# Performance work log

Measured on AMD Instinct MI355X. Metric: run time of the kernel, lower is better.

Reference implementation:

```python
import jax, jax.numpy as jnp
import numpy as np

V, E, H, T = 50000, 300, 512, 16   # vocab, embed_dim, hidden_dim, tagset
Hh = H // 2                         # per-direction LSTM hidden
B, S = 128, 128                     # batch (hardcoded in module), seq_len
START, STOP = 14, 15
NEG = -10000.0


def setup_inputs() -> dict:
    key = jax.random.key(0)
    ks = jax.random.split(key, 16)
    n = lambda k, sh: (jax.random.normal(k, sh, dtype=jnp.float32) * 0.1)
    trans = jax.random.normal(ks[12], (T, T), dtype=jnp.float32)
    trans = trans.at[START, :].set(NEG).at[:, STOP].set(NEG)
    return {
        "sentence": jax.random.randint(ks[0], (B, S), 0, V, dtype=jnp.int32),
        "emb": jax.random.normal(ks[1], (V, E), dtype=jnp.float32),
        "Wih_f": n(ks[2], (4 * Hh, E)), "Whh_f": n(ks[3], (4 * Hh, Hh)),
        "bih_f": n(ks[4], (4 * Hh,)),   "bhh_f": n(ks[5], (4 * Hh,)),
        "Wih_b": n(ks[6], (4 * Hh, E)), "Whh_b": n(ks[7], (4 * Hh, Hh)),
        "bih_b": n(ks[8], (4 * Hh,)),   "bhh_b": n(ks[9], (4 * Hh,)),
        "W_out": n(ks[10], (T, H)),     "b_out": n(ks[11], (T,)),
        "trans": trans,
        "h0": jax.random.normal(ks[13], (2, B, Hh), dtype=jnp.float32),
        "c0": jax.random.normal(ks[14], (2, B, Hh), dtype=jnp.float32),
    }


def _lstm_dir(x_sbE, h0, c0, Wih, Whh, bih, bhh):
    """x_sbE: [S,B,E] -> [S,B,Hh]. PyTorch gate order: i,f,g,o."""
    def cell(carry, xt):
        h, c = carry
        g = xt @ Wih.T + bih + h @ Whh.T + bhh
        i, f, gg, o = jnp.split(g, 4, axis=-1)
        c = jax.nn.sigmoid(f) * c + jax.nn.sigmoid(i) * jnp.tanh(gg)
        h = jax.nn.sigmoid(o) * jnp.tanh(c)
        return (h, c), h
    _, hs = jax.lax.scan(cell, (h0, c0), x_sbE)
    return hs


def _viterbi(feats, trans):
    """Batched Viterbi. feats: [B,S,T]. Returns (scores [B], paths [B,S])."""
    init = jnp.full((B, T), NEG, dtype=feats.dtype).at[:, START].set(0.0)

    def step(fv, feat_t):
        # next_tag_var[b, next, prev] = fv[b, prev] + trans[next, prev]
        nxt = fv[:, None, :] + trans[None, :, :]
        bp = jnp.argmax(nxt, axis=-1)              # [B,T]
        fv = jnp.max(nxt, axis=-1) + feat_t        # [B,T]
        return fv, bp

    fv, bps = jax.lax.scan(step, init, jnp.swapaxes(feats, 0, 1))  # bps: [S,B,T]
    term = fv + trans[STOP][None, :]
    best = jnp.argmax(term, axis=-1)               # [B]
    score = jnp.max(term, axis=-1)                 # [B]

    def back(tag, bp_t):
        prev = jnp.take_along_axis(bp_t, tag[:, None], axis=1)[:, 0]
        return prev, tag

    _, path = jax.lax.scan(back, best, bps, reverse=True)  # [S,B]
    return score, jnp.swapaxes(path, 0, 1)


def reference(sentence, emb, Wih_f, Whh_f, bih_f, bhh_f,
              Wih_b, Whh_b, bih_b, bhh_b, W_out, b_out, trans, h0, c0):
    x = emb[sentence]                               # [B,S,E] (frozen embedding)
    x_sbE = jnp.swapaxes(x, 0, 1)                   # [S,B,E]
    h_f = _lstm_dir(x_sbE, h0[0], c0[0], Wih_f, Whh_f, bih_f, bhh_f)
    h_b = _lstm_dir(x_sbE[::-1], h0[1], c0[1], Wih_b, Whh_b, bih_b, bhh_b)[::-1]
    lstm_out = jnp.concatenate([h_f, h_b], axis=-1)  # [S,B,H]
    feats = jnp.swapaxes(lstm_out @ W_out.T + b_out, 0, 1)  # [B,S,T]
    scores, tag_seqs = _viterbi(feats, trans)
    return scores, tag_seqs
```

## Files before the change

### kernel.cpp

```cpp
#include <hip/hip_runtime.h>
#include <math.h>

#define BB 128
#define SS 128
#define EE 300
#define HH 256
#define G4 1024
#define TT 16
#define NEGV -10000.0f
#define START_TAG 14
#define STOP_TAG 15

typedef float f32x4 __attribute__((ext_vector_type(4)));
typedef int   i32x4 __attribute__((ext_vector_type(4)));

__device__ __forceinline__ float sigm(float x) { return 1.0f / (1.0f + expf(-x)); }

__device__ __forceinline__ float4 shfl_xor4(float4 v, int m) {
  float4 r;
  r.x = __shfl_xor(v.x, m); r.y = __shfl_xor(v.y, m);
  r.z = __shfl_xor(v.z, m); r.w = __shfl_xor(v.w, m);
  return r;
}
__device__ __forceinline__ void add4(float4& a, const float4& b) {
  a.x += b.x; a.y += b.y; a.z += b.z; a.w += b.w;
}

__device__ __forceinline__ void load_f8_llc(const float* p, f32x4& a, f32x4& b) {
  asm volatile("global_load_dwordx4 %0, %2, off sc0 sc1\n\t"
               "global_load_dwordx4 %1, %2, off offset:16 sc0 sc1\n\t"
               "s_waitcnt vmcnt(0)"
               : "=&v"(a), "=&v"(b) : "v"(p) : "memory");
}
__device__ __forceinline__ void load_tags8(const int* p, i32x4& a, i32x4& b) {
  asm volatile("global_load_dwordx4 %0, %2, off sc0 sc1\n\t"
               "global_load_dwordx4 %1, %2, off offset:16 sc0 sc1\n\t"
               "s_waitcnt vmcnt(0)"
               : "=&v"(a), "=&v"(b) : "v"(p) : "memory");
}

__global__ void k_prep(const float* __restrict__ Wih_f, const float* __restrict__ Whh_f,
                       const float* __restrict__ bih_f, const float* __restrict__ bhh_f,
                       const float* __restrict__ Wih_b, const float* __restrict__ Whh_b,
                       const float* __restrict__ bih_b, const float* __restrict__ bhh_b,
                       float* __restrict__ WihT, float* __restrict__ Whh4,
                       float* __restrict__ bsum, int* __restrict__ ctr) {
  int id = blockIdx.x * blockDim.x + threadIdx.x;
  const int N1 = 2 * EE * G4;
  const int N2 = 2 * HH * G4;
  const int N3 = 2 * G4;
  if (id < N1) {
    int d = id / (EE * G4); int r = id % (EE * G4);
    int e = r / G4; int j = r % G4;
    const float* W = d ? Wih_b : Wih_f;
    WihT[id] = W[j * EE + e];
  } else if (id < N1 + N2) {
    int t = id - N1;
    int d = t / (HH * G4); int r = t % (HH * G4);
    int k = r / G4; int q = r % G4; int u = q >> 2; int g = q & 3;
    const float* W = d ? Whh_b : Whh_f;
    Whh4[t] = W[(g * HH + u) * HH + k];
  } else if (id < N1 + N2 + N3) {
    int t = id - N1 - N2;
    int d = t / G4; int j = t % G4;
    bsum[t] = d ? (bih_b[j] + bhh_b[j]) : (bih_f[j] + bhh_f[j]);
  } else if (id < N1 + N2 + N3 + 32 * 256) {
    ctr[id - N1 - N2 - N3] = 0;
  }
}

__global__ void k_xproj(const int* __restrict__ sent, const float* __restrict__ emb,
                        const float* __restrict__ WihT, const float* __restrict__ bsum,
                        float4* __restrict__ xp4) {
  __shared__ float xs[16][EE];
  __shared__ int idxs[16];
  int blk = blockIdx.x;
  int d = blk >> 10;
  int tile = blk & 1023;
  int tid = threadIdx.x;
  if (tid < 16) {
    int sb = tile * 16 + tid;
    int s = sb >> 7, b = sb & 127;
    idxs[tid] = sent[b * SS + s];
  }
  __syncthreads();
  for (int t = tid; t < 16 * EE; t += 256) {
    int i = t / EE, e = t % EE;
    xs[i][e] = emb[(size_t)idxs[i] * EE + e];
  }
  __syncthreads();

  const float* WT = WihT + (size_t)d * EE * G4;
  float acc0[16], acc1[16], acc2[16], acc3[16];
#pragma unroll
  for (int i = 0; i < 16; ++i) { acc0[i] = 0.f; acc1[i] = 0.f; acc2[i] = 0.f; acc3[i] = 0.f; }

  for (int e = 0; e < EE; ++e) {
    const float* row = WT + (size_t)e * G4;
    float w0 = row[tid];
    float w1 = row[tid + 256];
    float w2 = row[tid + 512];
    float w3 = row[tid + 768];
#pragma unroll
    for (int i = 0; i < 16; ++i) {
      float x = xs[i][e];
      acc0[i] += w0 * x; acc1[i] += w1 * x; acc2[i] += w2 * x; acc3[i] += w3 * x;
    }
  }
  float b0 = bsum[d * G4 + tid];
  float b1 = bsum[d * G4 + tid + 256];
  float b2 = bsum[d * G4 + tid + 512];
  float b3 = bsum[d * G4 + tid + 768];
#pragma unroll
  for (int i = 0; i < 16; ++i) {
    int sb = tile * 16 + i;
    int s = sb >> 7, b = sb & 127;
    xp4[(((size_t)d * SS + s) * BB + b) * HH + tid] =
        make_float4(acc0[i] + b0, acc1[i] + b1, acc2[i] + b2, acc3[i] + b3);
  }
}

__global__ __launch_bounds__(256, 1) void k_recur(
    const float4* __restrict__ xp4, const float4* __restrict__ Wg,
    const float* __restrict__ Wout, const float* __restrict__ h0,
    const float* __restrict__ c0, float* __restrict__ hbuf,
    float* __restrict__ featsP, int* __restrict__ ctr) {
  __shared__ __align__(16) float hshS[8 * 288];
  __shared__ float hloc[8 * 33];
  __shared__ float WoL[16 * 33];

  int blk = blockIdx.x;
  int d = blk >> 7;
  int bg = (blk >> 3) & 15;
  int sl = blk & 7;
  int bbase = bg * 8;
  int tid = threadIdx.x;
  int u = tid >> 3, kc = tid & 7;
  int uglob = sl * 32 + u;
  int* tagsg = ctr + (d * 16 + bg) * 256 + 64;

  for (int i = tid; i < 16 * 32; i += 256) {
    int t = i >> 5, uu = i & 31;
    WoL[t * 33 + uu] = Wout[t * 512 + d * HH + sl * 32 + uu];
  }

  float4 wreg[32];
  {
    const float4* Wd = Wg + (size_t)d * (HH * HH) + (size_t)(kc * 32) * HH + uglob;
#pragma unroll
    for (int kk = 0; kk < 32; ++kk) wreg[kk] = Wd[(size_t)kk * HH];
  }
  int b_own = ((kc & 1) << 2) | (kc & 2) | ((kc >> 2) & 1);
  float c_reg = c0[((size_t)d * BB + bbase + b_own) * HH + uglob];
  bool up0 = (kc & 1), up1 = (kc & 2), up2 = (kc & 4);

  float* ldst = hshS + (tid >> 5) * 288 + ((tid & 31) >> 2) * 36 + (tid & 3) * 8;

  for (int step = 0; step < SS; ++step) {
    int s = d ? (SS - 1 - step) : step;
    float4 xg = xp4[(((size_t)d * SS + s) * BB + bbase + b_own) * HH + uglob];

    if (step > 0) {
      i32x4 ta, tb;
      int m;
      do {
        load_tags8(tagsg, ta, tb);
        int m0 = min(min(ta[0], ta[1]), min(ta[2], ta[3]));
        int m1 = min(min(tb[0], tb[1]), min(tb[2], tb[3]));
        m = min(m0, m1);
      } while (m < step);
      const float* ps = hbuf + ((size_t)((step - 1) % 3) * 2 + d) * BB * HH +
                        (size_t)bbase * HH + (tid << 3);
      f32x4 a, b;
      load_f8_llc(ps, a, b);
      *(f32x4*)ldst = a;
      *(f32x4*)(ldst + 4) = b;
    } else {
      const float* ps = h0 + ((size_t)d * BB + bbase) * HH + (tid << 3);
      f32x4 a = *(const f32x4*)ps;
      f32x4 b = *(const f32x4*)(ps + 4);
      *(f32x4*)ldst = a;
      *(f32x4*)(ldst + 4) = b;
    }
    __syncthreads();

    float4 a[8];
#pragma unroll
    for (int b = 0; b < 8; ++b) a[b] = make_float4(0.f, 0.f, 0.f, 0.f);
#pragma unroll
    for (int kk4 = 0; kk4 < 8; ++kk4) {
      float hvv[8][4];
#pragma unroll
      for (int b = 0; b < 8; ++b)
        *(float4*)&hvv[b][0] = *(const float4*)&hshS[b * 288 + kc * 36 + kk4 * 4];
#pragma unroll
      for (int j = 0; j < 4; ++j) {
        float4 w = wreg[kk4 * 4 + j];
#pragma unroll
        for (int b = 0; b < 8; ++b) {
          float hj = hvv[b][j];
          a[b].x += w.x * hj; a[b].y += w.y * hj;
          a[b].z += w.z * hj; a[b].w += w.w * hj;
        }
      }
    }

#pragma unroll
    for (int j = 0; j < 4; ++j) {
      float4 snd = up0 ? a[j] : a[j + 4];
      float4 rcv = shfl_xor4(snd, 1);
      if (!up0) add4(a[j], rcv); else add4(a[j + 4], rcv);
    }
    float4 v0 = up0 ? a[4] : a[0];
    float4 v1 = up0 ? a[5] : a[1];
    float4 v2 = up0 ? a[6] : a[2];
    float4 v3 = up0 ? a[7] : a[3];
    {
      float4 snd = up1 ? v0 : v2;
      float4 rcv = shfl_xor4(snd, 2);
      if (!up1) add4(v0, rcv); else add4(v2, rcv);
      snd = up1 ? v1 : v3;
      rcv = shfl_xor4(snd, 2);
      if (!up1) add4(v1, rcv); else add4(v3, rcv);
    }
    float4 w0 = up1 ? v2 : v0;
    float4 w1 = up1 ? v3 : v1;
    {
      float4 snd = up2 ? w0 : w1;
      float4 rcv = shfl_xor4(snd, 4);
      if (!up2) add4(w0, rcv); else add4(w1, rcv);
    }
    float4 g4 = up2 ? w1 : w0;

    float ii = g4.x + xg.x, ff = g4.y + xg.y, gg = g4.z + xg.z, oo = g4.w + xg.w;
    c_reg = sigm(ff) * c_reg + sigm(ii) * tanhf(gg);
    float hn = sigm(oo) * tanhf(c_reg);

    __hip_atomic_store(
        &hbuf[((size_t)(step % 3) * 2 + d) * BB * HH + (size_t)(bbase + b_own) * HH + uglob],
        hn, __ATOMIC_RELAXED, __HIP_MEMORY_SCOPE_AGENT);
    hloc[b_own * 33 + u] = hn;
    __syncthreads();

    if (tid == 0)
      __hip_atomic_store(&tagsg[sl], step + 1, __ATOMIC_RELAXED,
                         __HIP_MEMORY_SCOPE_AGENT);

    {
      int b2 = tid >> 5, t = (tid >> 1) & 15, pr = tid & 1;
      float p = 0.f;
#pragma unroll
      for (int q = 0; q < 16; ++q)
        p += hloc[b2 * 33 + pr * 16 + q] * WoL[t * 33 + pr * 16 + q];
      p += __shfl_xor(p, 1);
      if (!pr)
        featsP[(((size_t)(d * 8 + sl) * BB + bbase + b2) * SS + s) * TT + t] = p;
    }
  }
}

__global__ void k_fsum(const float* __restrict__ featsP, float* __restrict__ featsF) {
  int b = blockIdx.x;
  int tid = threadIdx.x;
  float acc[8];
#pragma unroll
  for (int j = 0; j < 8; ++j) acc[j] = 0.f;
  for (int dsl = 0; dsl < 16; ++dsl) {
    const float* fp = featsP + ((size_t)dsl * BB + b) * (SS * TT);
#pragma unroll
    for (int j = 0; j < 8; ++j) acc[j] += fp[j * 256 + tid];
  }
  float* fo = featsF + (size_t)b * (SS * TT);
#pragma unroll
  for (int j = 0; j < 8; ++j) fo[j * 256 + tid] = acc[j];
}

__global__ void k_viterbi(const float* __restrict__ featsF, const float* __restrict__ b_out,
                          const float* __restrict__ trans, float* __restrict__ out,
                          unsigned char* __restrict__ bp) {
  __shared__ float tr[TT * TT];
  int tid = threadIdx.x;
  if (tid < TT * TT) tr[tid] = trans[tid];
  __syncthreads();

  int bg = tid >> 4;
  int next = tid & 15;
  int b = blockIdx.x * 16 + bg;
  float fv = (next == START_TAG) ? 0.0f : NEGV;
  float bo = b_out[next];
  const float* fF = featsF + (size_t)b * SS * TT;

  for (int s = 0; s < SS; ++s) {
    float best = -INFINITY; int arg = 0;
#pragma unroll
    for (int prev = 0; prev < TT; ++prev) {
      float fvp = __shfl(fv, prev, 16);
      float cand = fvp + tr[next * TT + prev];
      if (cand > best) { best = cand; arg = prev; }
    }
    float feat = fF[s * TT + next] + bo;
    fv = best + feat;
    bp[((size_t)b * SS + s) * TT + next] = (unsigned char)arg;
  }

  float bv = fv + tr[STOP_TAG * TT + next];
  int bi = next;
#pragma unroll
  for (int off = 8; off; off >>= 1) {
    float ov = __shfl_down(bv, off, 16);
    int oi = __shfl_down(bi, off, 16);
    if (ov > bv || (ov == bv && oi < bi)) { bv = ov; bi = oi; }
  }
  if (next == 0) {
    out[b] = bv;
    int tag = bi;
    float* po = out + BB + (size_t)b * SS;
    for (int s = SS - 1; s >= 0; --s) {
      po[s] = (float)tag;
      tag = bp[((size_t)b * SS + s) * TT + tag];
    }
  }
}

extern "C" void kernel_launch(void* const* d_in, const int* in_sizes, int n_in,
                              void* d_out, int out_size, void* d_ws, size_t ws_size,
                              hipStream_t stream) {
  const int*   sent  = (const int*)d_in[0];
  const float* emb   = (const float*)d_in[1];
  const float* Wih_f = (const float*)d_in[2];
  const float* Whh_f = (const float*)d_in[3];
  const float* bih_f = (const float*)d_in[4];
  const float* bhh_f = (const float*)d_in[5];
  const float* Wih_b = (const float*)d_in[6];
  const float* Whh_b = (const float*)d_in[7];
  const float* bih_b = (const float*)d_in[8];
  const float* bhh_b = (const float*)d_in[9];
  const float* Wout  = (const float*)d_in[10];
  const float* b_out = (const float*)d_in[11];
  const float* trans = (const float*)d_in[12];
  const float* h0    = (const float*)d_in[13];
  const float* c0    = (const float*)d_in[14];

  float* ws = (float*)d_ws;
  size_t off = 0;
  float* xproj  = ws + off; off += (size_t)2 * SS * BB * G4;
  float* WihT   = ws + off; off += (size_t)2 * EE * G4;
  float* Whh4   = ws + off; off += (size_t)2 * HH * G4;
  float* bsum   = ws + off; off += (size_t)2 * G4;
  float* featsP = ws + off; off += (size_t)16 * BB * SS * TT;
  float* featsF = ws + off; off += (size_t)BB * SS * TT;
  float* hbuf   = ws + off; off += (size_t)3 * 2 * BB * HH;
  int*   ctr    = (int*)(ws + off); off += 32 * 256;
  unsigned char* bp = (unsigned char*)(ws + off);

  const int NPREP = 2 * EE * G4 + 2 * HH * G4 + 2 * G4 + 32 * 256;
  k_prep<<<(NPREP + 255) / 256, 256, 0, stream>>>(Wih_f, Whh_f, bih_f, bhh_f,
                                                  Wih_b, Whh_b, bih_b, bhh_b,
                                                  WihT, Whh4, bsum, ctr);
  k_xproj<<<2048, 256, 0, stream>>>(sent, emb, WihT, bsum, (float4*)xproj);

  {
    const float4* xp4c = (const float4*)xproj;
    const float4* Wgc  = (const float4*)Whh4;
    void* kargs[] = {(void*)&xp4c, (void*)&Wgc, (void*)&Wout, (void*)&h0,
                     (void*)&c0, (void*)&hbuf, (void*)&featsP, (void*)&ctr};
    hipError_t e = hipLaunchCooperativeKernel(k_recur, dim3(256), dim3(256),
                                              kargs, 0, stream);
    if (e != hipSuccess) {
      k_recur<<<256, 256, 0, stream>>>(xp4c, Wgc, Wout, h0, c0, hbuf, featsP, ctr);
    }
  }

  k_fsum<<<BB, 256, 0, stream>>>(featsP, featsF);
  k_viterbi<<<8, 256, 0, stream>>>(featsF, b_out, trans, (float*)d_out, bp);
}
```

Measured before the change: 856.0 us.

## Split LSTM recurrence across twice as many blocks with 4 batches each

The recurrent kernel now uses 512 cooperative blocks, each handling 4 batch rows instead of 8, with launch bounds allowing two blocks per CU. This halves per-step FMA work and shuffle reduction depth per block to shorten the serial critical path. The cost is more inter-block flag traffic and duplicated weight registers. The input projection also switches to vectorized float4 embedding and shared-memory loads, and Viterbi backpointers move from global to shared memory.

```diff
diff --git a/kernel.cpp b/kernel.cpp
--- a/kernel.cpp
+++ b/kernel.cpp
@@ -1,5 +1,6 @@
 #include <hip/hip_runtime.h>
 #include <math.h>
+#include <stdint.h>
 
 #define BB 128
 #define SS 128
@@ -26,11 +27,12 @@
   a.x += b.x; a.y += b.y; a.z += b.z; a.w += b.w;
 }
 
-__device__ __forceinline__ void load_f8_llc(const float* p, f32x4& a, f32x4& b) {
-  asm volatile("global_load_dwordx4 %0, %2, off sc0 sc1\n\t"
-               "global_load_dwordx4 %1, %2, off offset:16 sc0 sc1\n\t"
+__device__ __forceinline__ f32x4 load_f4_llc(const float* p) {
+  f32x4 v;
+  asm volatile("global_load_dwordx4 %0, %1, off sc0 sc1\n\t"
                "s_waitcnt vmcnt(0)"
-               : "=&v"(a), "=&v"(b) : "v"(p) : "memory");
+               : "=v"(v) : "v"(p) : "memory");
+  return v;
 }
 __device__ __forceinline__ void load_tags8(const int* p, i32x4& a, i32x4& b) {
   asm volatile("global_load_dwordx4 %0, %2, off sc0 sc1\n\t"
@@ -49,6 +51,7 @@
   const int N1 = 2 * EE * G4;
   const int N2 = 2 * HH * G4;
   const int N3 = 2 * G4;
+  const int N4 = 64 * 256;
   if (id < N1) {
     int d = id / (EE * G4); int r = id % (EE * G4);
     int e = r / G4; int j = r % G4;
@@ -64,7 +67,7 @@
     int t = id - N1 - N2;
     int d = t / G4; int j = t % G4;
     bsum[t] = d ? (bih_b[j] + bhh_b[j]) : (bih_f[j] + bhh_f[j]);
-  } else if (id < N1 + N2 + N3 + 32 * 256) {
+  } else if (id < N1 + N2 + N3 + N4) {
     ctr[id - N1 - N2 - N3] = 0;
   }
 }
@@ -72,7 +75,7 @@
 __global__ void k_xproj(const int* __restrict__ sent, const float* __restrict__ emb,
                         const float* __restrict__ WihT, const float* __restrict__ bsum,
                         float4* __restrict__ xp4) {
-  __shared__ float xs[16][EE];
+  __shared__ __align__(16) float xs[16][EE];
   __shared__ int idxs[16];
   int blk = blockIdx.x;
   int d = blk >> 10;
@@ -84,9 +87,9 @@
     idxs[tid] = sent[b * SS + s];
   }
   __syncthreads();
-  for (int t = tid; t < 16 * EE; t += 256) {
-    int i = t / EE, e = t % EE;
-    xs[i][e] = emb[(size_t)idxs[i] * EE + e];
+  for (int t = tid; t < 16 * 75; t += 256) {
+    int i = t / 75, e4 = t % 75;
+    ((f32x4*)&xs[i][0])[e4] = ((const f32x4*)(emb + (size_t)idxs[i] * EE))[e4];
   }
   __syncthreads();
 
@@ -95,16 +98,24 @@
 #pragma unroll
   for (int i = 0; i < 16; ++i) { acc0[i] = 0.f; acc1[i] = 0.f; acc2[i] = 0.f; acc3[i] = 0.f; }
 
-  for (int e = 0; e < EE; ++e) {
-    const float* row = WT + (size_t)e * G4;
-    float w0 = row[tid];
-    float w1 = row[tid + 256];
-    float w2 = row[tid + 512];
-    float w3 = row[tid + 768];
-#pragma unroll
-    for (int i = 0; i < 16; ++i) {
-      float x = xs[i][e];
-      acc0[i] += w0 * x; acc1[i] += w1 * x; acc2[i] += w2 * x; acc3[i] += w3 * x;
+  for (int e4 = 0; e4 < 75; ++e4) {
+    f32x4 xv[16];
+#pragma unroll
+    for (int i = 0; i < 16; ++i)
+      xv[i] = *(const f32x4*)&xs[i][e4 * 4];
+    const float* rowb = WT + (size_t)e4 * 4 * G4;
+#pragma unroll
+    for (int j = 0; j < 4; ++j) {
+      const float* row = rowb + (size_t)j * G4;
+      float w0 = row[tid];
+      float w1 = row[tid + 256];
+      float w2 = row[tid + 512];
+      float w3 = row[tid + 768];
+#pragma unroll
+      for (int i = 0; i < 16; ++i) {
+        float x = xv[i][j];
+        acc0[i] += w0 * x; acc1[i] += w1 * x; acc2[i] += w2 * x; acc3[i] += w3 * x;
+      }
     }
   }
   float b0 = bsum[d * G4 + tid];
@@ -120,24 +131,24 @@
   }
 }
 
-__global__ __launch_bounds__(256, 1) void k_recur(
+__global__ __launch_bounds__(256, 2) void k_recur(
     const float4* __restrict__ xp4, const float4* __restrict__ Wg,
     const float* __restrict__ Wout, const float* __restrict__ h0,
     const float* __restrict__ c0, float* __restrict__ hbuf,
     float* __restrict__ featsP, int* __restrict__ ctr) {
-  __shared__ __align__(16) float hshS[8 * 288];
-  __shared__ float hloc[8 * 33];
+  __shared__ __align__(16) float hshS[4 * 288];
+  __shared__ float hloc[4 * 33];
   __shared__ float WoL[16 * 33];
 
   int blk = blockIdx.x;
-  int d = blk >> 7;
-  int bg = (blk >> 3) & 15;
+  int d = blk >> 8;
+  int bg = (blk >> 3) & 31;
   int sl = blk & 7;
-  int bbase = bg * 8;
+  int bbase = bg * 4;
   int tid = threadIdx.x;
   int u = tid >> 3, kc = tid & 7;
   int uglob = sl * 32 + u;
-  int* tagsg = ctr + (d * 16 + bg) * 256 + 64;
+  int* tagsg = ctr + (d * 32 + bg) * 256 + 64;
 
   for (int i = tid; i < 16 * 32; i += 256) {
     int t = i >> 5, uu = i & 31;
@@ -150,17 +161,23 @@
 #pragma unroll
     for (int kk = 0; kk < 32; ++kk) wreg[kk] = Wd[(size_t)kk * HH];
   }
-  int b_own = ((kc & 1) << 2) | (kc & 2) | ((kc >> 2) & 1);
+  int b_own = ((kc & 1) << 1) | ((kc >> 1) & 1);
   float c_reg = c0[((size_t)d * BB + bbase + b_own) * HH + uglob];
-  bool up0 = (kc & 1), up1 = (kc & 2), up2 = (kc & 4);
-
-  float* ldst = hshS + (tid >> 5) * 288 + ((tid & 31) >> 2) * 36 + (tid & 3) * 8;
+  bool up0 = (kc & 1), up1 = (kc & 2);
+
+  int sb = tid >> 6;
+  int sk = (tid & 63) * 4;
+  int ldoff = sb * 288 + (sk >> 5) * 36 + (sk & 31);
 
   for (int step = 0; step < SS; ++step) {
     int s = d ? (SS - 1 - step) : step;
     float4 xg = xp4[(((size_t)d * SS + s) * BB + bbase + b_own) * HH + uglob];
 
-    if (step > 0) {
+    float* ldst = &hshS[ldoff];
+    if (step == 0) {
+      const float* ps = h0 + ((size_t)d * BB + bbase + sb) * HH + sk;
+      *(f32x4*)ldst = *(const f32x4*)ps;
+    } else {
       i32x4 ta, tb;
       int m;
       do {
@@ -170,34 +187,25 @@
         m = min(m0, m1);
       } while (m < step);
       const float* ps = hbuf + ((size_t)((step - 1) % 3) * 2 + d) * BB * HH +
-                        (size_t)bbase * HH + (tid << 3);
-      f32x4 a, b;
-      load_f8_llc(ps, a, b);
-      *(f32x4*)ldst = a;
-      *(f32x4*)(ldst + 4) = b;
-    } else {
-      const float* ps = h0 + ((size_t)d * BB + bbase) * HH + (tid << 3);
-      f32x4 a = *(const f32x4*)ps;
-      f32x4 b = *(const f32x4*)(ps + 4);
-      *(f32x4*)ldst = a;
-      *(f32x4*)(ldst + 4) = b;
+                        (size_t)(bbase + sb) * HH + sk;
+      *(f32x4*)ldst = load_f4_llc(ps);
     }
     __syncthreads();
 
-    float4 a[8];
-#pragma unroll
-    for (int b = 0; b < 8; ++b) a[b] = make_float4(0.f, 0.f, 0.f, 0.f);
+    float4 a[4];
+#pragma unroll
+    for (int b = 0; b < 4; ++b) a[b] = make_float4(0.f, 0.f, 0.f, 0.f);
 #pragma unroll
     for (int kk4 = 0; kk4 < 8; ++kk4) {
-      float hvv[8][4];
-#pragma unroll
-      for (int b = 0; b < 8; ++b)
-        *(float4*)&hvv[b][0] = *(const float4*)&hshS[b * 288 + kc * 36 + kk4 * 4];
+      float hvv[4][4];
+#pragma unroll
+      for (int b = 0; b < 4; ++b)
+        *(f32x4*)&hvv[b][0] = *(const f32x4*)&hshS[b * 288 + kc * 36 + kk4 * 4];
 #pragma unroll
       for (int j = 0; j < 4; ++j) {
         float4 w = wreg[kk4 * 4 + j];
 #pragma unroll
-        for (int b = 0; b < 8; ++b) {
+        for (int b = 0; b < 4; ++b) {
           float hj = hvv[b][j];
           a[b].x += w.x * hj; a[b].y += w.y * hj;
           a[b].z += w.z * hj; a[b].w += w.w * hj;
@@ -206,40 +214,35 @@
     }
 
 #pragma unroll
-    for (int j = 0; j < 4; ++j) {
-      float4 snd = up0 ? a[j] : a[j + 4];
+    for (int j = 0; j < 2; ++j) {
+      float4 snd = up0 ? a[j] : a[j + 2];
       float4 rcv = shfl_xor4(snd, 1);
-      if (!up0) add4(a[j], rcv); else add4(a[j + 4], rcv);
-    }
-    float4 v0 = up0 ? a[4] : a[0];
-    float4 v1 = up0 ? a[5] : a[1];
-    float4 v2 = up0 ? a[6] : a[2];
-    float4 v3 = up0 ? a[7] : a[3];
+      if (!up0) add4(a[j], rcv); else add4(a[j + 2], rcv);
+    }
+    float4 v0 = up0 ? a[2] : a[0];
+    float4 v1 = up0 ? a[3] : a[1];
     {
-      float4 snd = up1 ? v0 : v2;
+      float4 snd = up1 ? v0 : v1;
       float4 rcv = shfl_xor4(snd, 2);
-      if (!up1) add4(v0, rcv); else add4(v2, rcv);
-      snd = up1 ? v1 : v3;
-      rcv = shfl_xor4(snd, 2);
-      if (!up1) add4(v1, rcv); else add4(v3, rcv);
-    }
-    float4 w0 = up1 ? v2 : v0;
-    float4 w1 = up1 ? v3 : v1;
+      if (!up1) add4(v0, rcv); else add4(v1, rcv);
+    }
+    float4 keep = up1 ? v1 : v0;
     {
-      float4 snd = up2 ? w0 : w1;
-      float4 rcv = shfl_xor4(snd, 4);
-      if (!up2) add4(w0, rcv); else add4(w1, rcv);
-    }
-    float4 g4 = up2 ? w1 : w0;
-
-    float ii = g4.x + xg.x, ff = g4.y + xg.y, gg = g4.z + xg.z, oo = g4.w + xg.w;
+      float4 rcv = shfl_xor4(keep, 4);
+      add4(keep, rcv);
+    }
+
+    float ii = keep.x + xg.x, ff = keep.y + xg.y;
+    float gg = keep.z + xg.z, oo = keep.w + xg.w;
     c_reg = sigm(ff) * c_reg + sigm(ii) * tanhf(gg);
     float hn = sigm(oo) * tanhf(c_reg);
 
-    __hip_atomic_store(
-        &hbuf[((size_t)(step % 3) * 2 + d) * BB * HH + (size_t)(bbase + b_own) * HH + uglob],
-        hn, __ATOMIC_RELAXED, __HIP_MEMORY_SCOPE_AGENT);
-    hloc[b_own * 33 + u] = hn;
+    if (kc < 4) {
+      __hip_atomic_store(
+          &hbuf[((size_t)(step % 3) * 2 + d) * BB * HH + (size_t)(bbase + b_own) * HH + uglob],
+          hn, __ATOMIC_RELAXED, __HIP_MEMORY_SCOPE_AGENT);
+      hloc[b_own * 33 + u] = hn;
+    }
     __syncthreads();
 
     if (tid == 0)
@@ -247,13 +250,14 @@
                          __HIP_MEMORY_SCOPE_AGENT);
 
     {
-      int b2 = tid >> 5, t = (tid >> 1) & 15, pr = tid & 1;
+      int b2 = tid >> 6, t = (tid >> 2) & 15, pr = tid & 3;
       float p = 0.f;
 #pragma unroll
-      for (int q = 0; q < 16; ++q)
-        p += hloc[b2 * 33 + pr * 16 + q] * WoL[t * 33 + pr * 16 + q];
+      for (int q = 0; q < 8; ++q)
+        p += hloc[b2 * 33 + pr * 8 + q] * WoL[t * 33 + pr * 8 + q];
       p += __shfl_xor(p, 1);
-      if (!pr)
+      p += __shfl_xor(p, 2);
+      if (pr == 0)
         featsP[(((size_t)(d * 8 + sl) * BB + bbase + b2) * SS + s) * TT + t] = p;
     }
   }
@@ -276,9 +280,9 @@
 }
 
 __global__ void k_viterbi(const float* __restrict__ featsF, const float* __restrict__ b_out,
-                          const float* __restrict__ trans, float* __restrict__ out,
-                          unsigned char* __restrict__ bp) {
+                          const float* __restrict__ trans, float* __restrict__ out) {
   __shared__ float tr[TT * TT];
+  __shared__ unsigned char bpl[16][SS][TT];
   int tid = threadIdx.x;
   if (tid < TT * TT) tr[tid] = trans[tid];
   __syncthreads();
@@ -300,7 +304,7 @@
     }
     float feat = fF[s * TT + next] + bo;
     fv = best + feat;
-    bp[((size_t)b * SS + s) * TT + next] = (unsigned char)arg;
+    bpl[bg][s][next] = (unsigned char)arg;
   }
 
   float bv = fv + tr[STOP_TAG * TT + next];
@@ -317,7 +321,7 @@
     float* po = out + BB + (size_t)b * SS;
     for (int s = SS - 1; s >= 0; --s) {
       po[s] = (float)tag;
-      tag = bp[((size_t)b * SS + s) * TT + tag];
+      tag = bpl[bg][s][tag];
     }
   }
 }
@@ -350,10 +354,9 @@
   float* featsP = ws + off; off += (size_t)16 * BB * SS * TT;
   float* featsF = ws + off; off += (size_t)BB * SS * TT;
   float* hbuf   = ws + off; off += (size_t)3 * 2 * BB * HH;
-  int*   ctr    = (int*)(ws + off); off += 32 * 256;
-  unsigned char* bp = (unsigned char*)(ws + off);
-
-  const int NPREP = 2 * EE * G4 + 2 * HH * G4 + 2 * G4 + 32 * 256;
+  int*   ctr    = (int*)(ws + off); off += 64 * 256;
+
+  const int NPREP = 2 * EE * G4 + 2 * HH * G4 + 2 * G4 + 64 * 256;
   k_prep<<<(NPREP + 255) / 256, 256, 0, stream>>>(Wih_f, Whh_f, bih_f, bhh_f,
                                                   Wih_b, Whh_b, bih_b, bhh_b,
                                                   WihT, Whh4, bsum, ctr);
@@ -364,13 +367,13 @@
     const float4* Wgc  = (const float4*)Whh4;
     void* kargs[] = {(void*)&xp4c, (void*)&Wgc, (void*)&Wout, (void*)&h0,
                      (void*)&c0, (void*)&hbuf, (void*)&featsP, (void*)&ctr};
-    hipError_t e = hipLaunchCooperativeKernel(k_recur, dim3(256), dim3(256),
+    hipError_t e = hipLaunchCooperativeKernel(k_recur, dim3(512), dim3(256),
                                               kargs, 0, stream);
     if (e != hipSuccess) {
-      k_recur<<<256, 256, 0, stream>>>(xp4c, Wgc, Wout, h0, c0, hbuf, featsP, ctr);
+      k_recur<<<512, 256, 0, stream>>>(xp4c, Wgc, Wout, h0, c0, hbuf, featsP, ctr);
     }
   }
 
   k_fsum<<<BB, 256, 0, stream>>>(featsP, featsF);
-  k_viterbi<<<8, 256, 0, stream>>>(featsF, b_out, trans, (float*)d_out, bp);
-}
+  k_viterbi<<<8, 256, 0, stream>>>(featsF, b_out, trans, (float*)d_out);
+}
```

Measured after the change: 841.3 us. Within noise of the previous version (-1.7%).

## Fuse input projection into recurrent kernel with per-row readiness stamps

Applied to the files above, without the earlier changes.

Merges the x-projection GEMM and the LSTM recurrence into one launch. The first 256 blocks run the recurrence, and the remaining 2048 blocks compute input projections, ordered so forward and backward timesteps are produced in the order the recurrence consumes them. Each recurrent block spin-waits on a per-row stamp before reading its xproj slice, so the projection overlaps with the serial recurrence instead of running entirely before it. Viterbi backpointers also move from global memory into shared memory. The risks are forward-progress deadlock if the recurrent blocks are not all resident (the launch is no longer cooperative), plus polling overhead and contention between the two kinds of block.

```diff
diff --git a/kernel.cpp b/kernel.cpp
--- a/kernel.cpp
+++ b/kernel.cpp
@@ -1,5 +1,6 @@
 #include <hip/hip_runtime.h>
 #include <math.h>
+#include <stdint.h>
 
 #define BB 128
 #define SS 128
@@ -10,6 +11,8 @@
 #define NEGV -10000.0f
 #define START_TAG 14
 #define STOP_TAG 15
+#define NRB 256
+#define NXT 2048
 
 typedef float f32x4 __attribute__((ext_vector_type(4)));
 typedef int   i32x4 __attribute__((ext_vector_type(4)));
@@ -38,17 +41,38 @@
                "s_waitcnt vmcnt(0)"
                : "=&v"(a), "=&v"(b) : "v"(p) : "memory");
 }
+__device__ __forceinline__ f32x4 load_f4_llc(const float* p) {
+  f32x4 v;
+  asm volatile("global_load_dwordx4 %0, %1, off sc0 sc1\n\t"
+               "s_waitcnt vmcnt(0)"
+               : "=v"(v) : "v"(p) : "memory");
+  return v;
+}
+__device__ __forceinline__ int load_int_llc(const int* p) {
+  int v;
+  asm volatile("global_load_dword %0, %1, off sc0 sc1\n\t"
+               "s_waitcnt vmcnt(0)"
+               : "=v"(v) : "v"(p) : "memory");
+  return v;
+}
+__device__ __forceinline__ void store_f2_llc(float* p, float a, float b) {
+  uint64_t bits = ((uint64_t)__float_as_uint(b) << 32) | (uint64_t)__float_as_uint(a);
+  __hip_atomic_store((uint64_t*)p, bits, __ATOMIC_RELAXED, __HIP_MEMORY_SCOPE_AGENT);
+}
 
 __global__ void k_prep(const float* __restrict__ Wih_f, const float* __restrict__ Whh_f,
                        const float* __restrict__ bih_f, const float* __restrict__ bhh_f,
                        const float* __restrict__ Wih_b, const float* __restrict__ Whh_b,
                        const float* __restrict__ bih_b, const float* __restrict__ bhh_b,
                        float* __restrict__ WihT, float* __restrict__ Whh4,
-                       float* __restrict__ bsum, int* __restrict__ ctr) {
+                       float* __restrict__ bsum, int* __restrict__ ctr,
+                       int* __restrict__ xstamp) {
   int id = blockIdx.x * blockDim.x + threadIdx.x;
   const int N1 = 2 * EE * G4;
   const int N2 = 2 * HH * G4;
   const int N3 = 2 * G4;
+  const int N4 = 32 * 256;
+  const int N5 = 2 * SS * BB * 8;
   if (id < N1) {
     int d = id / (EE * G4); int r = id % (EE * G4);
     int e = r / G4; int j = r % G4;
@@ -64,197 +88,215 @@
     int t = id - N1 - N2;
     int d = t / G4; int j = t % G4;
     bsum[t] = d ? (bih_b[j] + bhh_b[j]) : (bih_f[j] + bhh_f[j]);
-  } else if (id < N1 + N2 + N3 + 32 * 256) {
+  } else if (id < N1 + N2 + N3 + N4) {
     ctr[id - N1 - N2 - N3] = 0;
-  }
-}
-
-__global__ void k_xproj(const int* __restrict__ sent, const float* __restrict__ emb,
-                        const float* __restrict__ WihT, const float* __restrict__ bsum,
-                        float4* __restrict__ xp4) {
-  __shared__ float xs[16][EE];
-  __shared__ int idxs[16];
-  int blk = blockIdx.x;
-  int d = blk >> 10;
-  int tile = blk & 1023;
-  int tid = threadIdx.x;
-  if (tid < 16) {
-    int sb = tile * 16 + tid;
-    int s = sb >> 7, b = sb & 127;
-    idxs[tid] = sent[b * SS + s];
-  }
-  __syncthreads();
-  for (int t = tid; t < 16 * EE; t += 256) {
-    int i = t / EE, e = t % EE;
-    xs[i][e] = emb[(size_t)idxs[i] * EE + e];
-  }
-  __syncthreads();
-
-  const float* WT = WihT + (size_t)d * EE * G4;
-  float acc0[16], acc1[16], acc2[16], acc3[16];
-#pragma unroll
-  for (int i = 0; i < 16; ++i) { acc0[i] = 0.f; acc1[i] = 0.f; acc2[i] = 0.f; acc3[i] = 0.f; }
-
-  for (int e = 0; e < EE; ++e) {
-    const float* row = WT + (size_t)e * G4;
-    float w0 = row[tid];
-    float w1 = row[tid + 256];
-    float w2 = row[tid + 512];
-    float w3 = row[tid + 768];
-#pragma unroll
-    for (int i = 0; i < 16; ++i) {
-      float x = xs[i][e];
-      acc0[i] += w0 * x; acc1[i] += w1 * x; acc2[i] += w2 * x; acc3[i] += w3 * x;
-    }
-  }
-  float b0 = bsum[d * G4 + tid];
-  float b1 = bsum[d * G4 + tid + 256];
-  float b2 = bsum[d * G4 + tid + 512];
-  float b3 = bsum[d * G4 + tid + 768];
-#pragma unroll
-  for (int i = 0; i < 16; ++i) {
-    int sb = tile * 16 + i;
-    int s = sb >> 7, b = sb & 127;
-    xp4[(((size_t)d * SS + s) * BB + b) * HH + tid] =
-        make_float4(acc0[i] + b0, acc1[i] + b1, acc2[i] + b2, acc3[i] + b3);
-  }
-}
-
-__global__ __launch_bounds__(256, 1) void k_recur(
-    const float4* __restrict__ xp4, const float4* __restrict__ Wg,
-    const float* __restrict__ Wout, const float* __restrict__ h0,
-    const float* __restrict__ c0, float* __restrict__ hbuf,
-    float* __restrict__ featsP, int* __restrict__ ctr) {
-  __shared__ __align__(16) float hshS[8 * 288];
+  } else if (id < N1 + N2 + N3 + N4 + N5) {
+    xstamp[id - N1 - N2 - N3 - N4] = 0;
+  }
+}
+
+__global__ __launch_bounds__(256, 2) void k_main(
+    const float4* __restrict__ Wg, const float* __restrict__ Wout,
+    const float* __restrict__ h0, const float* __restrict__ c0,
+    float* __restrict__ hbuf, float* __restrict__ featsP, int* __restrict__ ctr,
+    float* __restrict__ xp4, int* __restrict__ xstamp,
+    const int* __restrict__ sent, const float* __restrict__ emb,
+    const float* __restrict__ WihT, const float* __restrict__ bsum) {
+  __shared__ __align__(16) float smem[4800];
   __shared__ float hloc[8 * 33];
   __shared__ float WoL[16 * 33];
-
-  int blk = blockIdx.x;
-  int d = blk >> 7;
-  int bg = (blk >> 3) & 15;
-  int sl = blk & 7;
-  int bbase = bg * 8;
-  int tid = threadIdx.x;
-  int u = tid >> 3, kc = tid & 7;
-  int uglob = sl * 32 + u;
-  int* tagsg = ctr + (d * 16 + bg) * 256 + 64;
-
-  for (int i = tid; i < 16 * 32; i += 256) {
-    int t = i >> 5, uu = i & 31;
-    WoL[t * 33 + uu] = Wout[t * 512 + d * HH + sl * 32 + uu];
-  }
-
-  float4 wreg[32];
-  {
-    const float4* Wd = Wg + (size_t)d * (HH * HH) + (size_t)(kc * 32) * HH + uglob;
-#pragma unroll
-    for (int kk = 0; kk < 32; ++kk) wreg[kk] = Wd[(size_t)kk * HH];
-  }
-  int b_own = ((kc & 1) << 2) | (kc & 2) | ((kc >> 2) & 1);
-  float c_reg = c0[((size_t)d * BB + bbase + b_own) * HH + uglob];
-  bool up0 = (kc & 1), up1 = (kc & 2), up2 = (kc & 4);
-
-  float* ldst = hshS + (tid >> 5) * 288 + ((tid & 31) >> 2) * 36 + (tid & 3) * 8;
-
-  for (int step = 0; step < SS; ++step) {
-    int s = d ? (SS - 1 - step) : step;
-    float4 xg = xp4[(((size_t)d * SS + s) * BB + bbase + b_own) * HH + uglob];
-
-    if (step > 0) {
-      i32x4 ta, tb;
-      int m;
-      do {
-        load_tags8(tagsg, ta, tb);
-        int m0 = min(min(ta[0], ta[1]), min(ta[2], ta[3]));
-        int m1 = min(min(tb[0], tb[1]), min(tb[2], tb[3]));
-        m = min(m0, m1);
-      } while (m < step);
-      const float* ps = hbuf + ((size_t)((step - 1) % 3) * 2 + d) * BB * HH +
-                        (size_t)bbase * HH + (tid << 3);
-      f32x4 a, b;
-      load_f8_llc(ps, a, b);
-      *(f32x4*)ldst = a;
-      *(f32x4*)(ldst + 4) = b;
-    } else {
-      const float* ps = h0 + ((size_t)d * BB + bbase) * HH + (tid << 3);
-      f32x4 a = *(const f32x4*)ps;
-      f32x4 b = *(const f32x4*)(ps + 4);
-      *(f32x4*)ldst = a;
-      *(f32x4*)(ldst + 4) = b;
+  __shared__ int idxs[16];
+  int blk = blockIdx.x, tid = threadIdx.x;
+
+  if (blk < NRB) {
+    int d = blk >> 7, bg = (blk >> 3) & 15, sl = blk & 7;
+    int bbase = bg * 8;
+    int u = tid >> 3, kc = tid & 7;
+    int uglob = sl * 32 + u;
+    int* tagsg = ctr + (d * 16 + bg) * 256 + 64;
+
+    for (int i = tid; i < 16 * 32; i += 256) {
+      int t = i >> 5, uu = i & 31;
+      WoL[t * 33 + uu] = Wout[t * 512 + d * HH + sl * 32 + uu];
+    }
+
+    float4 wreg[32];
+    {
+      const float4* Wd = Wg + (size_t)d * (HH * HH) + (size_t)(kc * 32) * HH + uglob;
+#pragma unroll
+      for (int kk = 0; kk < 32; ++kk) wreg[kk] = Wd[(size_t)kk * HH];
+    }
+    int b_own = ((kc & 1) << 2) | (kc & 2) | ((kc >> 2) & 1);
+    float c_reg = c0[((size_t)d * BB + bbase + b_own) * HH + uglob];
+    bool up0 = (kc & 1), up1 = (kc & 2), up2 = (kc & 4);
+
+    float* ldst = &smem[(tid >> 5) * 288 + ((tid & 31) >> 2) * 36 + (tid & 3) * 8];
+
+    for (int step = 0; step < SS; ++step) {
+      int s = d ? (SS - 1 - step) : step;
+
+      float4 xg;
+      {
+        const int* sp = xstamp + ((size_t)(d * SS + s) * BB + bbase + b_own) * 8 + sl;
+        while (load_int_llc(sp) != 1) __builtin_amdgcn_s_sleep(4);
+        f32x4 xv = load_f4_llc(xp4 + ((size_t)(d * SS + s) * BB + bbase + b_own) * G4 +
+                               uglob * 4);
+        xg = make_float4(xv[0], xv[1], xv[2], xv[3]);
+      }
+
+      if (step == 0) {
+        const float* ps = h0 + ((size_t)d * BB + bbase) * HH + (tid << 3);
+        *(f32x4*)ldst = *(const f32x4*)ps;
+        *(f32x4*)(ldst + 4) = *(const f32x4*)(ps + 4);
+      } else {
+        i32x4 ta, tb;
+        int m;
+        do {
+          load_tags8(tagsg, ta, tb);
+          int m0 = min(min(ta[0], ta[1]), min(ta[2], ta[3]));
+          int m1 = min(min(tb[0], tb[1]), min(tb[2], tb[3]));
+          m = min(m0, m1);
+        } while (m < step);
+        const float* ps = hbuf + ((size_t)((step - 1) % 3) * 2 + d) * BB * HH +
+                          (size_t)bbase * HH + (tid << 3);
+        f32x4 a, b;
+        load_f8_llc(ps, a, b);
+        *(f32x4*)ldst = a;
+        *(f32x4*)(ldst + 4) = b;
+      }
+      __syncthreads();
+
+      float4 a[8];
+#pragma unroll
+      for (int b = 0; b < 8; ++b) a[b] = make_float4(0.f, 0.f, 0.f, 0.f);
+#pragma unroll
+      for (int kk4 = 0; kk4 < 8; ++kk4) {
+        float hvv[8][4];
+#pragma unroll
+        for (int b = 0; b < 8; ++b)
+          *(f32x4*)&hvv[b][0] = *(const f32x4*)&smem[b * 288 + kc * 36 + kk4 * 4];
+#pragma unroll
+        for (int j = 0; j < 4; ++j) {
+          float4 w = wreg[kk4 * 4 + j];
+#pragma unroll
+          for (int b = 0; b < 8; ++b) {
+            float hj = hvv[b][j];
+            a[b].x += w.x * hj; a[b].y += w.y * hj;
+            a[b].z += w.z * hj; a[b].w += w.w * hj;
+          }
+        }
+      }
+
+#pragma unroll
+      for (int j = 0; j < 4; ++j) {
+        float4 snd = up0 ? a[j] : a[j + 4];
+        float4 rcv = shfl_xor4(snd, 1);
+        if (!up0) add4(a[j], rcv); else add4(a[j + 4], rcv);
+      }
+      float4 v0 = up0 ? a[4] : a[0];
+      float4 v1 = up0 ? a[5] : a[1];
+      float4 v2 = up0 ? a[6] : a[2];
+      float4 v3 = up0 ? a[7] : a[3];
+      {
+        float4 snd = up1 ? v0 : v2;
+        float4 rcv = shfl_xor4(snd, 2);
+        if (!up1) add4(v0, rcv); else add4(v2, rcv);
+        snd = up1 ? v1 : v3;
+        rcv = shfl_xor4(snd, 2);
+        if (!up1) add4(v1, rcv); else add4(v3, rcv);
+      }
+      float4 w0 = up1 ? v2 : v0;
+      float4 w1 = up1 ? v3 : v1;
+      {
+        float4 snd = up2 ? w0 : w1;
+        float4 rcv = shfl_xor4(snd, 4);
+        if (!up2) add4(w0, rcv); else add4(w1, rcv);
+      }
+      float4 g4 = up2 ? w1 : w0;
+
+      float ii = g4.x + xg.x, ff = g4.y + xg.y, gg = g4.z + xg.z, oo = g4.w + xg.w;
+      c_reg = sigm(ff) * c_reg + sigm(ii) * tanhf(gg);
+      float hn = sigm(oo) * tanhf(c_reg);
+
+      __hip_atomic_store(
+          &hbuf[((size_t)(step % 3) * 2 + d) * BB * HH + (size_t)(bbase + b_own) * HH + uglob],
+          hn, __ATOMIC_RELAXED, __HIP_MEMORY_SCOPE_AGENT);
+      hloc[b_own * 33 + u] = hn;
+      __syncthreads();
+
+      if (tid == 0)
+        __hip_atomic_store(&tagsg[sl], step + 1, __ATOMIC_RELAXED,
+                           __HIP_MEMORY_SCOPE_AGENT);
+
+      {
+        int b2 = tid >> 5, t = (tid >> 1) & 15, pr = tid & 1;
+        float p = 0.f;
+#pragma unroll
+        for (int q = 0; q < 16; ++q)
+          p += hloc[b2 * 33 + pr * 16 + q] * WoL[t * 33 + pr * 16 + q];
+        p += __shfl_xor(p, 1);
+        if (!pr)
+          featsP[(((size_t)(d * 8 + sl) * BB + bbase + b2) * SS + s) * TT + t] = p;
+      }
+    }
+  } else {
+    int xb = blk - NRB;
+    int d = xb & 1;
+    int t16 = xb >> 1;
+    int t = d ? (1023 - t16) : t16;
+
+    if (tid < 16) {
+      int sb = t * 16 + tid;
+      int s = sb >> 7, b = sb & 127;
+      idxs[tid] = sent[b * SS + s];
     }
     __syncthreads();
-
-    float4 a[8];
-#pragma unroll
-    for (int b = 0; b < 8; ++b) a[b] = make_float4(0.f, 0.f, 0.f, 0.f);
-#pragma unroll
-    for (int kk4 = 0; kk4 < 8; ++kk4) {
-      float hvv[8][4];
-#pragma unroll
-      for (int b = 0; b < 8; ++b)
-        *(float4*)&hvv[b][0] = *(const float4*)&hshS[b * 288 + kc * 36 + kk4 * 4];
+    for (int i = tid; i < 16 * 75; i += 256) {
+      int r = i / 75, e4 = i % 75;
+      *(f32x4*)&smem[r * 300 + e4 * 4] = ((const f32x4*)(emb + (size_t)idxs[r] * EE))[e4];
+    }
+    __syncthreads();
+
+    const float* WT = WihT + (size_t)d * EE * G4;
+    float acc0[16], acc1[16], acc2[16], acc3[16];
+#pragma unroll
+    for (int i = 0; i < 16; ++i) { acc0[i] = 0.f; acc1[i] = 0.f; acc2[i] = 0.f; acc3[i] = 0.f; }
+
+    for (int e4 = 0; e4 < 75; ++e4) {
+      const float* rowb = WT + (size_t)e4 * 4 * G4;
 #pragma unroll
       for (int j = 0; j < 4; ++j) {
-        float4 w = wreg[kk4 * 4 + j];
-#pragma unroll
-        for (int b = 0; b < 8; ++b) {
-          float hj = hvv[b][j];
-          a[b].x += w.x * hj; a[b].y += w.y * hj;
-          a[b].z += w.z * hj; a[b].w += w.w * hj;
+        const float* row = rowb + (size_t)j * G4;
+        float w0 = row[tid];
+        float w1 = row[tid + 256];
+        float w2 = row[tid + 512];
+        float w3 = row[tid + 768];
+#pragma unroll
+        for (int i = 0; i < 16; ++i) {
+          float x = smem[i * 300 + e4 * 4 + j];
+          acc0[i] += w0 * x; acc1[i] += w1 * x; acc2[i] += w2 * x; acc3[i] += w3 * x;
         }
       }
     }
-
-#pragma unroll
-    for (int j = 0; j < 4; ++j) {
-      float4 snd = up0 ? a[j] : a[j + 4];
-      float4 rcv = shfl_xor4(snd, 1);
-      if (!up0) add4(a[j], rcv); else add4(a[j + 4], rcv);
-    }
-    float4 v0 = up0 ? a[4] : a[0];
-    float4 v1 = up0 ? a[5] : a[1];
-    float4 v2 = up0 ? a[6] : a[2];
-    float4 v3 = up0 ? a[7] : a[3];
-    {
-      float4 snd = up1 ? v0 : v2;
-      float4 rcv = shfl_xor4(snd, 2);
-      if (!up1) add4(v0, rcv); else add4(v2, rcv);
-      snd = up1 ? v1 : v3;
-      rcv = shfl_xor4(snd, 2);
-      if (!up1) add4(v1, rcv); else add4(v3, rcv);
-    }
-    float4 w0 = up1 ? v2 : v0;
-    float4 w1 = up1 ? v3 : v1;
-    {
-      float4 snd = up2 ? w0 : w1;
-      float4 rcv = shfl_xor4(snd, 4);
-      if (!up2) add4(w0, rcv); else add4(w1, rcv);
-    }
-    float4 g4 = up2 ? w1 : w0;
-
-    float ii = g4.x + xg.x, ff = g4.y + xg.y, gg = g4.z + xg.z, oo = g4.w + xg.w;
-    c_reg = sigm(ff) * c_reg + sigm(ii) * tanhf(gg);
-    float hn = sigm(oo) * tanhf(c_reg);
-
-    __hip_atomic_store(
-        &hbuf[((size_t)(step % 3) * 2 + d) * BB * HH + (size_t)(bbase + b_own) * HH + uglob],
-        hn, __ATOMIC_RELAXED, __HIP_MEMORY_SCOPE_AGENT);
-    hloc[b_own * 33 + u] = hn;
+    float b0 = bsum[d * G4 + tid];
+    float b1 = bsum[d * G4 + tid + 256];
+    float b2 = bsum[d * G4 + tid + 512];
+    float b3 = bsum[d * G4 + tid + 768];
+#pragma unroll
+    for (int i = 0; i < 16; ++i) {
+      int sb = t * 16 + i;
+      int s = sb >> 7, b = sb & 127;
+      float* base = xp4 + ((size_t)(d * SS + s) * BB + b) * G4 + tid * 4;
+      store_f2_llc(base, acc0[i] + b0, acc1[i] + b1);
+      store_f2_llc(base + 2, acc2[i] + b2, acc3[i] + b3);
+    }
     __syncthreads();
-
-    if (tid == 0)
-      __hip_atomic_store(&tagsg[sl], step + 1, __ATOMIC_RELAXED,
-                         __HIP_MEMORY_SCOPE_AGENT);
-
-    {
-      int b2 = tid >> 5, t = (tid >> 1) & 15, pr = tid & 1;
-      float p = 0.f;
-#pragma unroll
-      for (int q = 0; q < 16; ++q)
-        p += hloc[b2 * 33 + pr * 16 + q] * WoL[t * 33 + pr * 16 + q];
-      p += __shfl_xor(p, 1);
-      if (!pr)
-        featsP[(((size_t)(d * 8 + sl) * BB + bbase + b2) * SS + s) * TT + t] = p;
+    if (tid < 128) {
+      int r = tid >> 3, sl = tid & 7;
+      int sb = t * 16 + r;
+      int s = sb >> 7, b = sb & 127;
+      __hip_atomic_store(xstamp + ((size_t)(d * SS + s) * BB + b) * 8 + sl, 1,
+                         __ATOMIC_RELAXED, __HIP_MEMORY_SCOPE_AGENT);
     }
   }
 }
@@ -276,9 +318,9 @@
 }
 
 __global__ void k_viterbi(const float* __restrict__ featsF, const float* __restrict__ b_out,
-                          const float* __restrict__ trans, float* __restrict__ out,
-                          unsigned char* __restrict__ bp) {
+                          const float* __restrict__ trans, float* __restrict__ out) {
   __shared__ float tr[TT * TT];
+  __shared__ unsigned char bpl[16][SS][TT];
   int tid = threadIdx.x;
   if (tid < TT * TT) tr[tid] = trans[tid];
   __syncthreads();
@@ -300,7 +342,7 @@
     }
     float feat = fF[s * TT + next] + bo;
     fv = best + feat;
-    bp[((size_t)b * SS + s) * TT + next] = (unsigned char)arg;
+    bpl[bg][s][next] = (unsigned char)arg;
   }
 
   float bv = fv + tr[STOP_TAG * TT + next];
@@ -317,7 +359,7 @@
     float* po = out + BB + (size_t)b * SS;
     for (int s = SS - 1; s >= 0; --s) {
       po[s] = (float)tag;
-      tag = bp[((size_t)b * SS + s) * TT + tag];
+      tag = bpl[bg][s][tag];
     }
   }
 }
@@ -343,7 +385,8 @@
 
   float* ws = (float*)d_ws;
   size_t off = 0;
-  float* xproj  = ws + off; off += (size_t)2 * SS * BB * G4;
+  float* xp4    = ws + off; off += (size_t)2 * SS * BB * G4;
+  int*   xstamp = (int*)(ws + off); off += (size_t)2 * SS * BB * 8;
   float* WihT   = ws + off; off += (size_t)2 * EE * G4;
   float* Whh4   = ws + off; off += (size_t)2 * HH * G4;
   float* bsum   = ws + off; off += (size_t)2 * G4;
@@ -351,26 +394,16 @@
   float* featsF = ws + off; off += (size_t)BB * SS * TT;
   float* hbuf   = ws + off; off += (size_t)3 * 2 * BB * HH;
   int*   ctr    = (int*)(ws + off); off += 32 * 256;
-  unsigned char* bp = (unsigned char*)(ws + off);
-
-  const int NPREP = 2 * EE * G4 + 2 * HH * G4 + 2 * G4 + 32 * 256;
+
+  const int NPREP = 2 * EE * G4 + 2 * HH * G4 + 2 * G4 + 32 * 256 + 2 * SS * BB * 8;
   k_prep<<<(NPREP + 255) / 256, 256, 0, stream>>>(Wih_f, Whh_f, bih_f, bhh_f,
                                                   Wih_b, Whh_b, bih_b, bhh_b,
-                                                  WihT, Whh4, bsum, ctr);
-  k_xproj<<<2048, 256, 0, stream>>>(sent, emb, WihT, bsum, (float4*)xproj);
-
-  {
-    const float4* xp4c = (const float4*)xproj;
-    const float4* Wgc  = (const float4*)Whh4;
-    void* kargs[] = {(void*)&xp4c, (void*)&Wgc, (void*)&Wout, (void*)&h0,
-                     (void*)&c0, (void*)&hbuf, (void*)&featsP, (void*)&ctr};
-    hipError_t e = hipLaunchCooperativeKernel(k_recur, dim3(256), dim3(256),
-                                              kargs, 0, stream);
-    if (e != hipSuccess) {
-      k_recur<<<256, 256, 0, stream>>>(xp4c, Wgc, Wout, h0, c0, hbuf, featsP, ctr);
-    }
-  }
+                                                  WihT, Whh4, bsum, ctr, xstamp);
+
+  k_main<<<NRB + NXT, 256, 0, stream>>>((const float4*)Whh4, Wout, h0, c0,
+                                        hbuf, featsP, ctr, xp4, xstamp,
+                                        sent, emb, WihT, bsum);
 
   k_fsum<<<BB, 256, 0, stream>>>(featsP, featsF);
-  k_viterbi<<<8, 256, 0, stream>>>(featsF, b_out, trans, (float*)d_out, bp);
-}
+  k_viterbi<<<8, 256, 0, stream>>>(featsF, b_out, trans, (float*)d_out);
+}
```

Measured after the change: 1.173 ms. 1.37x slower.
